# Optimization experiments

Measured on AMD Instinct MI355X. Metric: run time of the kernel, lower is better.

## Reference

```python
import jax, jax.numpy as jnp
import numpy as np
from jax import lax

NF, CF, LAT = 128, 3, 512          # n_filter, sobel c_factor (id+gx+gy), lat_size
NL, NC = 3, 4                      # n_layers (img 64 -> 3), n_calls
B, IMG, CH = 16, 64, 3
FIN, FH, FOUT = NF * CF, NF, 2 * NF  # dyna/res block in, hidden, out (gated -> 2*NF)
SPLIT = [NF, NF, NF, 1]
NOUT = sum(SPLIT)                  # 385
CS = NF + NF * 16 + NF * 16 + 16 * 16  # 4480 multi-cut state size
SEG = [FIN * FH, FH, FH * FH, FH, FH * FOUT, FOUT, FIN * FOUT, FOUT]
OFF = np.concatenate([[0], np.cumsum(SEG)]).astype(int)
K = int(OFF[-1])                   # hypernet output size (197376)

SOBEL_X = jnp.array([[-1., 0., 1.], [-2., 0., 2.], [-1., 0., 1.]], jnp.float32) / 8.0
SOBEL_Y = SOBEL_X.T
_g = np.exp(-0.5 * (np.arange(3) - 1.0) ** 2); _g /= _g.sum()
GAUSS = jnp.asarray(np.outer(_g, _g), jnp.float32)  # 3x3 gaussian, sigma=1


def dwconv(x, k2d):
    # depthwise conv, same 3x3 kernel for every channel, padding 1
    C = x.shape[1]
    k = jnp.broadcast_to(k2d.astype(x.dtype), (C, 1, 3, 3))
    return lax.conv_general_dilated(x, k, (1, 1), ((1, 1), (1, 1)),
                                    dimension_numbers=('NCHW', 'OIHW', 'NCHW'),
                                    feature_group_count=C)


def instnorm(x, eps=1e-5):
    m = x.mean((2, 3), keepdims=True)
    v = x.var((2, 3), keepdims=True)
    return (x - m) * lax.rsqrt(v + eps)


def conv1x1(x, w, b):  # w: [O, C]
    return jnp.einsum('bchw,oc->bohw', x, w) + b[None, :, None, None]


def lrb(x, w1, b1, w2, b2, wsc, bsc):  # LinearResidualBlock
    return x @ wsc.T + bsc + jax.nn.relu(x @ w1.T + b1) @ w2.T + b2


def _w(k, shape, fan_in):
    return jax.random.normal(k, shape, jnp.float32) / np.sqrt(fan_in)


def setup_inputs():
    ks = jax.random.split(jax.random.key(0), 24)
    z = lambda *s: jnp.zeros(s, jnp.float32)
    d = {}
    d['x'] = jax.random.normal(ks[0], (B, CH, IMG, IMG), jnp.float32)
    d['inj_lat'] = jax.random.normal(ks[1], (B, LAT), jnp.float32)
    d['leak_factor'] = jnp.float32(0.1)
    d['in_w'] = _w(ks[2], (NF, CH), CH); d['in_b'] = z(NF)
    d['fc_w1'] = _w(ks[3], (FH, FIN), FIN); d['fc_b1'] = z(FH)
    d['fc_w2'] = _w(ks[4], (FOUT, FH), FH); d['fc_b2'] = z(FOUT)
    d['fc_wsc'] = _w(ks[5], (FOUT, FIN), FIN); d['fc_bsc'] = z(FOUT)
    d['hyp_w'] = _w(ks[6], (K, LAT), LAT) * 0.1; d['hyp_b'] = z(K)
    d['lat_w'] = _w(ks[7], (NL * NC, LAT, LAT), LAT); d['lat_b'] = z(NL * NC, LAT)
    d['seed'] = _w(ks[8], (1, NF, 16, 16), NF)
    d['out_w'] = _w(ks[9], (NOUT, NF), NF); d['out_b'] = z(NOUT)
    d['l1_w1'] = _w(ks[10], (2 * LAT, CS), CS); d['l1_b1'] = z(2 * LAT)
    d['l1_w2'] = _w(ks[11], (LAT, 2 * LAT), 2 * LAT); d['l1_b2'] = z(LAT)
    d['l1_wsc'] = _w(ks[12], (LAT, CS), CS); d['l1_bsc'] = z(LAT)
    d['l2_w1'] = _w(ks[13], (LAT, LAT), LAT); d['l2_b1'] = z(LAT)
    d['l2_w2'] = _w(ks[14], (LAT, LAT), LAT); d['l2_b2'] = z(LAT)
    d['l2_wsc'] = _w(ks[15], (LAT, LAT), LAT); d['l2_bsc'] = z(LAT)
    d['fin_w'] = _w(ks[16], (LAT, LAT), LAT); d['fin_b'] = z(LAT)
    return d


def _forward(x, inj_lat, leak_factor, in_w, in_b, fc_w1, fc_b1, fc_w2, fc_b2,
             fc_wsc, fc_bsc, hyp_w, hyp_b, lat_w, lat_b, seed, out_w, out_b,
             l1_w1, l1_b1, l1_w2, l1_b2, l1_wsc, l1_bsc,
             l2_w1, l2_b1, l2_w2, l2_b2, l2_wsc, l2_bsc, fin_w, fin_b):
    out = conv1x1(x, in_w, in_b)
    leak = jnp.clip(leak_factor, 0.001, 1000.0)
    for c in range(NL * NC):
        # perception: identity + x/y sobel (c_factor=3), then instance norm
        p = jnp.concatenate([out, dwconv(out, SOBEL_X), dwconv(out, SOBEL_Y)], 1)
        p = instnorm(p)
        # static ResidualBlock (shared params)
        f = conv1x1(p, fc_wsc, fc_bsc) + conv1x1(jax.nn.relu(conv1x1(p, fc_w1, fc_b1)), fc_w2, fc_b2)
        # per-call latent expansion + hypernetwork -> per-sample 1x1 conv weights
        latc = inj_lat @ lat_w[c].T + lat_b[c]
        hk = latc @ hyp_w.T + hyp_b  # [B, K]
        w_in = hk[:, OFF[0]:OFF[1]].reshape(-1, FH, FIN); b_in = hk[:, OFF[1]:OFF[2]]
        w_md = hk[:, OFF[2]:OFF[3]].reshape(-1, FH, FH);  b_md = hk[:, OFF[3]:OFF[4]]
        w_ot = hk[:, OFF[4]:OFF[5]].reshape(-1, FOUT, FH); b_ot = hk[:, OFF[5]:OFF[6]]
        w_sc = hk[:, OFF[6]:OFF[7]].reshape(-1, FOUT, FIN); b_sc = hk[:, OFF[7]:OFF[8]]
        h = jax.nn.relu(jnp.einsum('bchw,boc->bohw', p, w_in) + b_in[:, :, None, None])
        h = jax.nn.relu(jnp.einsum('bchw,boc->bohw', h, w_md) + b_md[:, :, None, None])
        d = (jnp.einsum('bchw,boc->bohw', p, w_sc) + b_sc[:, :, None, None]
             + jnp.einsum('bchw,boc->bohw', h, w_ot) + b_ot[:, :, None, None])
        out_new = f + d  # [B, 2*NF, H, W]
        a, g = out_new[:, :NF], out_new[:, NF:]
        out = out + leak * (a * jax.nn.sigmoid(g))
        if c < NL * NC - 1 and c % NC == NC - 1:
            s = dwconv(out, GAUSS)
            # bilinear 0.5 downscale (align_corners=False) == 2x2 average
            Bn, C, H, W = s.shape
            out = s.reshape(Bn, C, H // 2, 2, W // 2, 2).mean((3, 5))
    out = out + seed  # broadcast seed [1, NF, 16, 16]
    o = conv1x1(out, out_w, out_b)  # [B, 385, 16, 16]
    f_, fh_, fw_, hw_ = o[:, :NF], o[:, NF:2 * NF], o[:, 2 * NF:3 * NF], o[:, 3 * NF:]
    bs = o.shape[0]
    cs = jnp.concatenate([f_.mean((2, 3)), fh_.mean(3).reshape(bs, -1),
                          fw_.mean(2).reshape(bs, -1), hw_.reshape(bs, -1)], 1)  # [B, 4480]
    hcs = lrb(cs, l1_w1, l1_b1, l1_w2, l1_b2, l1_wsc, l1_bsc)
    hcs = lrb(hcs, l2_w1, l2_b1, l2_w2, l2_b2, l2_wsc, l2_bsc)
    return hcs @ fin_w.T + fin_b  # [B, LAT]


def reference(x, inj_lat, leak_factor, in_w, in_b, fc_w1, fc_b1, fc_w2, fc_b2,
              fc_wsc, fc_bsc, hyp_w, hyp_b, lat_w, lat_b, seed, out_w, out_b,
              l1_w1, l1_b1, l1_w2, l1_b2, l1_wsc, l1_bsc,
              l2_w1, l2_b1, l2_w2, l2_b2, l2_wsc, l2_bsc, fin_w, fin_b):
    return _forward(x, inj_lat, leak_factor, in_w, in_b, fc_w1, fc_b1, fc_w2, fc_b2,
                    fc_wsc, fc_bsc, hyp_w, hyp_b, lat_w, lat_b, seed, out_w, out_b,
                    l1_w1, l1_b1, l1_w2, l1_b2, l1_wsc, l1_bsc,
                    l2_w1, l2_b1, l2_w2, l2_b2, l2_wsc, l2_bsc, fin_w, fin_b)
```

## Files before the change

### kernel.cpp

```cpp
#include <hip/hip_runtime.h>
#include <hip/hip_bf16.h>

typedef __hip_bfloat16 bf16;
typedef __attribute__((ext_vector_type(8))) short bf8_t;
typedef __attribute__((ext_vector_type(4))) float f4_t;

#define KHK 197376
#define OFF_WIN 0
#define OFF_BIN 49152
#define OFF_WMD 49280
#define OFF_BMD 65664
#define OFF_WOT 65792
#define OFF_BOT 98560
#define OFF_WSC 98816
#define OFF_BSC 197120

__device__ __forceinline__ float ldf(const float* p, size_t i){ return p[i]; }
__device__ __forceinline__ float ldf(const bf16* p, size_t i){ return __bfloat162float(p[i]); }
__device__ __forceinline__ void stf(float* p, size_t i, float v){ p[i] = v; }
__device__ __forceinline__ void stf(bf16* p, size_t i, float v){ p[i] = __float2bfloat16(v); }
__device__ __forceinline__ float b2f(short u){ return __uint_as_float(((unsigned)(unsigned short)u) << 16); }

typedef const __attribute__((address_space(1))) unsigned int* gas_t;
typedef __attribute__((address_space(3))) unsigned int* las_t;
__device__ __forceinline__ void gld_lds16(const void* g, void* l){
  __builtin_amdgcn_global_load_lds((gas_t)g, (las_t)l, 16, 0, 0);
}

struct Seg { const bf16* p; int klen; int ld; };

__global__ __launch_bounds__(256) void k_cvt_bf16(const float* __restrict__ in,
    bf16* __restrict__ out, size_t n){
  size_t stride = (size_t)gridDim.x * 256;
  for (size_t i = blockIdx.x*256ULL + threadIdx.x; i*8 < n; i += stride){
    float4 a = *reinterpret_cast<const float4*>(in + i*8);
    float4 c = *reinterpret_cast<const float4*>(in + i*8 + 4);
    union { bf8_t v; bf16 e[8]; } o;
    o.e[0]=__float2bfloat16(a.x); o.e[1]=__float2bfloat16(a.y);
    o.e[2]=__float2bfloat16(a.z); o.e[3]=__float2bfloat16(a.w);
    o.e[4]=__float2bfloat16(c.x); o.e[5]=__float2bfloat16(c.y);
    o.e[6]=__float2bfloat16(c.z); o.e[7]=__float2bfloat16(c.w);
    *reinterpret_cast<bf8_t*>(out + i*8) = o.v;
  }
}

__global__ __launch_bounds__(256) void k_in_conv(const float* __restrict__ x,
    const float* __restrict__ w, const float* __restrict__ b, float* __restrict__ out){
  int idx = blockIdx.x*256 + threadIdx.x;
  int c = idx & 127;
  int s = (idx >> 7) & 4095;
  int bi = idx >> 19;
  const float* xb = x + (size_t)bi*3*4096;
  out[idx] = b[c] + w[c*3]*xb[s] + w[c*3+1]*xb[4096+s] + w[c*3+2]*xb[8192+s];
}

__global__ __launch_bounds__(256) void k_sobel4(const float* __restrict__ src,
    bf16* __restrict__ p, int H, int S){
  int idx = blockIdx.x*256 + threadIdx.x;
  int c4 = (idx & 31) * 4;
  int s = (idx >> 5) % S;
  int b = idx / (S*32);
  int y = s / H, x = s - y*H;
  const float* sb = src + (size_t)b*S*128 + c4;
  float4 n[3][3];
  #pragma unroll
  for (int dy=0; dy<3; dy++)
    #pragma unroll
    for (int dx=0; dx<3; dx++){
      int yy = y + dy - 1, xx = x + dx - 1;
      if (yy>=0 && yy<H && xx>=0 && xx<H)
        n[dy][dx] = *reinterpret_cast<const float4*>(sb + (size_t)(yy*H+xx)*128);
      else
        n[dy][dx] = (float4){0.f,0.f,0.f,0.f};
    }
  float v0[4], sx[4], sy[4];
  #pragma unroll
  for (int q = 0; q < 4; q++){
    float e00=((const float*)&n[0][0])[q], e01=((const float*)&n[0][1])[q], e02=((const float*)&n[0][2])[q];
    float e10=((const float*)&n[1][0])[q], e11=((const float*)&n[1][1])[q], e12=((const float*)&n[1][2])[q];
    float e20=((const float*)&n[2][0])[q], e21=((const float*)&n[2][1])[q], e22=((const float*)&n[2][2])[q];
    v0[q] = e11;
    sx[q] = (-e00 + e02 - 2.f*e10 + 2.f*e12 - e20 + e22) * 0.125f;
    sy[q] = (-e00 - 2.f*e01 - e02 + e20 + 2.f*e21 + e22) * 0.125f;
  }
  bf16* pb = p + ((size_t)b*S + s)*384;
  union { unsigned long long u; bf16 e[4]; } o0, o1, o2;
  #pragma unroll
  for (int q = 0; q < 4; q++){
    o0.e[q] = __float2bfloat16(v0[q]);
    o1.e[q] = __float2bfloat16(sx[q]);
    o2.e[q] = __float2bfloat16(sy[q]);
  }
  *reinterpret_cast<unsigned long long*>(pb + c4)       = o0.u;
  *reinterpret_cast<unsigned long long*>(pb + 128 + c4) = o1.u;
  *reinterpret_cast<unsigned long long*>(pb + 256 + c4) = o2.u;
}

__global__ __launch_bounds__(256) void k_stats(const bf16* __restrict__ P_,
    float* __restrict__ SUMS, int S){
  __shared__ float sS[384], sQ[384];
  int b = blockIdx.y;
  int chunk = S >> 4;
  int s0 = blockIdx.x * chunk;
  int t = threadIdx.x;
  for (int i = t; i < 384; i += 256){ sS[i] = 0.f; sQ[i] = 0.f; }
  __syncthreads();
  if (t < 240){
    int oct = t % 48, ls = t / 48;
    int c8 = oct*8;
    float as[8] = {}, qs[8] = {};
    for (int s = s0 + ls; s < s0 + chunk; s += 5){
      bf8_t v = *reinterpret_cast<const bf8_t*>(P_ + ((size_t)b*S + s)*384 + c8);
      #pragma unroll
      for (int i=0;i<8;i++){ float f = b2f(v[i]); as[i]+=f; qs[i]+=f*f; }
    }
    #pragma unroll
    for (int i=0;i<8;i++){ atomicAdd(&sS[c8+i], as[i]); atomicAdd(&sQ[c8+i], qs[i]); }
  }
  __syncthreads();
  for (int i = t; i < 384; i += 256){
    atomicAdd(&SUMS[((size_t)b*384+i)*2],   sS[i]);
    atomicAdd(&SUMS[((size_t)b*384+i)*2+1], sQ[i]);
  }
}

__global__ __launch_bounds__(256) void k_hyper_all(const float* __restrict__ hw,
    const float* __restrict__ hb, const bf16* __restrict__ latb,
    bf16* __restrict__ hk_all){
  __shared__ float Sw[128][17];
  int h0 = blockIdx.x * 128;
  int tid = threadIdx.x, wid = tid >> 6, lane = tid & 63;
  int lr = lane & 15, lg = lane >> 4;
  f4_t acc[2][12];
  #pragma unroll
  for (int f=0; f<2; f++)
    #pragma unroll
    for (int j=0; j<12; j++) acc[f][j] = (f4_t){0.f,0.f,0.f,0.f};
  for (int k0 = 0; k0 < 512; k0 += 32){
    bf8_t af[2];
    #pragma unroll
    for (int f = 0; f < 2; f++){
      int h = h0 + wid*32 + f*16 + lr;
      const float* src = hw + (size_t)h*512 + k0 + lg*8;
      float4 x0 = *reinterpret_cast<const float4*>(src);
      float4 x1 = *reinterpret_cast<const float4*>(src + 4);
      union { bf8_t v; bf16 e[8]; } o;
      o.e[0]=__float2bfloat16(x0.x); o.e[1]=__float2bfloat16(x0.y);
      o.e[2]=__float2bfloat16(x0.z); o.e[3]=__float2bfloat16(x0.w);
      o.e[4]=__float2bfloat16(x1.x); o.e[5]=__float2bfloat16(x1.y);
      o.e[6]=__float2bfloat16(x1.z); o.e[7]=__float2bfloat16(x1.w);
      af[f] = o.v;
    }
    #pragma unroll
    for (int j = 0; j < 12; j++){
      bf8_t bv = *reinterpret_cast<const bf8_t*>(latb + (size_t)(j*16 + lr)*512 + k0 + lg*8);
      acc[0][j] = __builtin_amdgcn_mfma_f32_16x16x32_bf16(af[0], bv, acc[0][j], 0, 0, 0);
      acc[1][j] = __builtin_amdgcn_mfma_f32_16x16x32_bf16(af[1], bv, acc[1][j], 0, 0, 0);
    }
  }
  for (int j = 0; j < 12; j++){
    __syncthreads();
    #pragma unroll
    for (int f = 0; f < 2; f++)
      #pragma unroll
      for (int r = 0; r < 4; r++)
        Sw[wid*32 + f*16 + lg*4 + r][lr] = acc[f][j][r];
    __syncthreads();
    int bb = tid >> 4, h8 = (tid & 15) * 8;
    union { bf8_t v; bf16 e[8]; } o;
    #pragma unroll
    for (int i = 0; i < 8; i++)
      o.e[i] = __float2bfloat16(hb[h0 + h8 + i] + Sw[h8 + i][bb]);
    *reinterpret_cast<bf8_t*>(hk_all + ((size_t)j*16 + bb)*KHK + h0 + h8) = o.v;
  }
}

__global__ __launch_bounds__(256) void k_latall(const float* __restrict__ inj,
    const float* __restrict__ lat_w, const float* __restrict__ lat_b,
    bf16* __restrict__ LATB){
  int gwave = (int)((blockIdx.x*256 + threadIdx.x) >> 6);
  int lane = threadIdx.x & 63;
  int c = gwave >> 9, o = gwave & 511;
  const float* wr = lat_w + (size_t)c*262144 + (size_t)o*512;
  float acc[16] = {};
  for (int k = lane; k < 512; k += 64){
    float wv = wr[k];
    #pragma unroll
    for (int b = 0; b < 16; b++) acc[b] += wv * inj[b*512 + k];
  }
  #pragma unroll
  for (int b = 0; b < 16; b++)
    for (int off = 32; off > 0; off >>= 1) acc[b] += __shfl_down(acc[b], off);
  if (lane == 0){
    float bv = lat_b[c*512 + o];
    #pragma unroll
    for (int b = 0; b < 16; b++)
      LATB[(size_t)c*8192 + b*512 + o] = __float2bfloat16(acc[b] + bv);
  }
}

__global__ __launch_bounds__(256) void k_xform(
    const float* __restrict__ fc_w1, const float* __restrict__ fc_b1,
    const float* __restrict__ fc_w2, const float* __restrict__ fc_b2,
    const float* __restrict__ fc_wsc, const float* __restrict__ fc_bsc,
    const bf16* __restrict__ HK_, const float* __restrict__ SUMS, float Sf,
    bf16* __restrict__ Wstack, float* __restrict__ bstack,
    bf16* __restrict__ Wbig, float* __restrict__ bbig,
    bf16* __restrict__ Wmd, float* __restrict__ bmd){
  int gw = (blockIdx.x*256 + threadIdx.x) >> 6;
  int lane = threadIdx.x & 63;
  float invSf = 1.f / Sf;
  if (gw < 4096){
    int b = gw >> 8, o = gw & 255;
    const float* su = SUMS + (size_t)b*768;
    const bf16* hkb = HK_ + (size_t)b*KHK;
    float b0 = (o < 128) ? fc_b1[o] : ldf(hkb, OFF_BIN + (o-128));
    float accv = 0.f;
    bf16* dst = Wstack + ((size_t)b*256 + o)*384;
    for (int k = lane; k < 384; k += 64){
      float m = su[k*2] * invSf;
      float iv = rsqrtf(fmaxf(su[k*2+1]*invSf - m*m, 0.f) + 1e-5f);
      float wv = (o < 128) ? fc_w1[(size_t)o*384 + k]
                           : ldf(hkb, OFF_WIN + (size_t)(o-128)*384 + k);
      float w = wv * iv;
      accv += w * m;
      dst[k] = __float2bfloat16(w);
    }
    for (int off=32; off>0; off>>=1) accv += __shfl_down(accv, off);
    if (lane==0) bstack[b*256+o] = b0 - accv;
  } else if (gw < 8192){
    int r = gw - 4096; int b = r >> 8, o = r & 255;
    const float* su = SUMS + (size_t)b*768;
    const bf16* hkb = HK_ + (size_t)b*KHK;
    int cc = o & 127;
    int nr = ((cc >> 4) << 5) + ((o >> 7) << 4) + (cc & 15);
    bf16* dst = Wbig + ((size_t)b*256 + nr)*640;
    float accv = 0.f;
    for (int k = lane; k < 384; k += 64){
      float m = su[k*2] * invSf;
      float iv = rsqrtf(fmaxf(su[k*2+1]*invSf - m*m, 0.f) + 1e-5f);
      float w = (fc_wsc[(size_t)o*384 + k] + ldf(hkb, OFF_WSC + (size_t)o*384 + k)) * iv;
      accv += w * m;
      dst[k] = __float2bfloat16(w);
    }
    for (int k = lane; k < 128; k += 64){
      dst[384+k] = __float2bfloat16(fc_w2[(size_t)o*128 + k]);
      dst[512+k] = hkb[OFF_WOT + (size_t)o*128 + k];
    }
    for (int off=32; off>0; off>>=1) accv += __shfl_down(accv, off);
    if (lane==0) bbig[b*256+nr] = fc_bsc[o] + ldf(hkb, OFF_BSC+o) + fc_b2[o]
                                  + ldf(hkb, OFF_BOT+o) - accv;
  } else {
    int r = gw - 8192; int b = r >> 7, o = r & 127;
    const bf16* hkb = HK_ + (size_t)b*KHK;
    bf16* dst = Wmd + ((size_t)b*128 + o)*128;
    for (int k = lane; k < 128; k += 64)
      dst[k] = hkb[OFF_WMD + (size_t)o*128 + k];
    if (lane==0) bmd[b*128+o] = ldf(hkb, OFF_BMD + o);
  }
}

__global__ __launch_bounds__(512) void k_gemm1(const bf16* __restrict__ P_,
    const bf16* __restrict__ W, const float* __restrict__ bias,
    bf16* __restrict__ HGo, int S){
  __shared__ short As[128][32];
  __shared__ short Bs[256][32];
  int b = blockIdx.z, s0 = blockIdx.x * 128;
  int tid = threadIdx.x, wid = tid >> 6, lane = tid & 63;
  int wrow = (wid >> 2) * 64, wcol = (wid & 3) * 64;
  int lr = lane & 15, lg = lane >> 4;
  int r0 = tid >> 2, c8 = (tid & 3) * 8;
  const bf16* Wb = W + (size_t)b * 98304;
  f4_t acc[4][4] = {{}};
  const bf16* gA  = P_ + ((size_t)b*S + s0 + r0) * 384 + c8;
  const bf16* gB0 = Wb + (size_t)r0 * 384 + c8;
  const bf16* gB1 = Wb + (size_t)(128 + r0) * 384 + c8;
  for (int k0 = 0; k0 < 384; k0 += 32){
    gld_lds16(gA + k0,  &As[wid*16][0]);
    gld_lds16(gB0 + k0, &Bs[wid*16][0]);
    gld_lds16(gB1 + k0, &Bs[128 + wid*16][0]);
    __syncthreads();
    bf8_t af[4], bfv[4];
    #pragma unroll
    for (int i = 0; i < 4; i++) af[i]  = *(const bf8_t*)(&As[wrow + i*16 + lr][lg*8]);
    #pragma unroll
    for (int j = 0; j < 4; j++) bfv[j] = *(const bf8_t*)(&Bs[wcol + j*16 + lr][lg*8]);
    #pragma unroll
    for (int i = 0; i < 4; i++)
      #pragma unroll
      for (int j = 0; j < 4; j++)
        acc[i][j] = __builtin_amdgcn_mfma_f32_16x16x32_bf16(af[i], bfv[j], acc[i][j], 0, 0, 0);
    __syncthreads();
  }
  #pragma unroll
  for (int j = 0; j < 4; j++){
    int n = wcol + j*16 + lr;
    float bv = bias[(size_t)b * 256 + n];
    #pragma unroll
    for (int i = 0; i < 4; i++){
      int sr = s0 + wrow + i*16 + lg*4;
      size_t base = ((size_t)b * S + sr) * 256 + n;
      #pragma unroll
      for (int r = 0; r < 4; r++)
        stf(HGo, base + (size_t)r * 256, fmaxf(acc[i][j][r] + bv, 0.f));
    }
  }
}

__global__ __launch_bounds__(512) void k_gemm23(
    const bf16* __restrict__ P_, const bf16* __restrict__ HG_,
    const bf16* __restrict__ Wmd, const float* __restrict__ bmd,
    const bf16* __restrict__ Wbig, const float* __restrict__ bbig,
    float* __restrict__ OUTf, int S, const float* __restrict__ leakp){
  __shared__ short As[128][32];
  __shared__ short Bs[256][32];
  __shared__ short G2t[128][136];
  int b = blockIdx.z, s0 = blockIdx.x * 128;
  int tid = threadIdx.x, wid = tid >> 6, lane = tid & 63;
  int lr = lane & 15, lg = lane >> 4;
  int r0 = tid >> 2, c8 = (tid & 3) * 8;
  bf16* G2b = (bf16*)&G2t[0][0];
  {
    int wrowA = (wid >> 1) * 32, wcolA = (wid & 1) * 64;
    f4_t accA[2][4] = {{}};
    const bf16* gA = HG_ + ((size_t)b*S + s0 + r0) * 256 + 128 + c8;
    const bf16* gB = Wmd + (size_t)b*16384 + (size_t)r0 * 128 + c8;
    for (int k0 = 0; k0 < 128; k0 += 32){
      gld_lds16(gA + k0, &As[wid*16][0]);
      gld_lds16(gB + k0, &Bs[wid*16][0]);
      __syncthreads();
      bf8_t af[2], bfv[4];
      #pragma unroll
      for (int i = 0; i < 2; i++) af[i]  = *(const bf8_t*)(&As[wrowA + i*16 + lr][lg*8]);
      #pragma unroll
      for (int j = 0; j < 4; j++) bfv[j] = *(const bf8_t*)(&Bs[wcolA + j*16 + lr][lg*8]);
      #pragma unroll
      for (int i = 0; i < 2; i++)
        #pragma unroll
        for (int j = 0; j < 4; j++)
          accA[i][j] = __builtin_amdgcn_mfma_f32_16x16x32_bf16(af[i], bfv[j], accA[i][j], 0, 0, 0);
      __syncthreads();
    }
    const float* bmdb = bmd + b*128;
    #pragma unroll
    for (int j = 0; j < 4; j++){
      int col = wcolA + j*16 + lr;
      float bv = bmdb[col];
      #pragma unroll
      for (int i = 0; i < 2; i++){
        int row = wrowA + i*16 + lg*4;
        #pragma unroll
        for (int r = 0; r < 4; r++)
          stf(G2b, (size_t)(row + r)*136 + col, fmaxf(accA[i][j][r] + bv, 0.f));
      }
    }
    __syncthreads();
  }
  int wrow = (wid >> 2) * 64, wcol = (wid & 3) * 64;
  f4_t acc[4][4] = {{}};
  const bf16* Wb = Wbig + (size_t)b * 163840;
  {
    const bf16* gA  = P_ + ((size_t)b*S + s0 + r0) * 384 + c8;
    const bf16* gB0 = Wb + (size_t)r0 * 640 + c8;
    const bf16* gB1 = Wb + (size_t)(128 + r0) * 640 + c8;
    for (int k0 = 0; k0 < 384; k0 += 32){
      gld_lds16(gA + k0,  &As[wid*16][0]);
      gld_lds16(gB0 + k0, &Bs[wid*16][0]);
      gld_lds16(gB1 + k0, &Bs[128 + wid*16][0]);
      __syncthreads();
      bf8_t af[4], bfv[4];
      #pragma unroll
      for (int i = 0; i < 4; i++) af[i]  = *(const bf8_t*)(&As[wrow + i*16 + lr][lg*8]);
      #pragma unroll
      for (int j = 0; j < 4; j++) bfv[j] = *(const bf8_t*)(&Bs[wcol + j*16 + lr][lg*8]);
      #pragma unroll
      for (int i = 0; i < 4; i++)
        #pragma unroll
        for (int j = 0; j < 4; j++)
          acc[i][j] = __builtin_amdgcn_mfma_f32_16x16x32_bf16(af[i], bfv[j], acc[i][j], 0, 0, 0);
      __syncthreads();
    }
  }
  {
    const bf16* gA  = HG_ + ((size_t)b*S + s0 + r0) * 256 + c8;
    const bf16* gB0 = Wb + (size_t)r0 * 640 + 384 + c8;
    const bf16* gB1 = Wb + (size_t)(128 + r0) * 640 + 384 + c8;
    for (int k0 = 0; k0 < 128; k0 += 32){
      gld_lds16(gA + k0,  &As[wid*16][0]);
      gld_lds16(gB0 + k0, &Bs[wid*16][0]);
      gld_lds16(gB1 + k0, &Bs[128 + wid*16][0]);
      __syncthreads();
      bf8_t af[4], bfv[4];
      #pragma unroll
      for (int i = 0; i < 4; i++) af[i]  = *(const bf8_t*)(&As[wrow + i*16 + lr][lg*8]);
      #pragma unroll
      for (int j = 0; j < 4; j++) bfv[j] = *(const bf8_t*)(&Bs[wcol + j*16 + lr][lg*8]);
      #pragma unroll
      for (int i = 0; i < 4; i++)
        #pragma unroll
        for (int j = 0; j < 4; j++)
          acc[i][j] = __builtin_amdgcn_mfma_f32_16x16x32_bf16(af[i], bfv[j], acc[i][j], 0, 0, 0);
      __syncthreads();
    }
  }
  {
    const bf16* gB0 = Wb + (size_t)r0 * 640 + 512 + c8;
    const bf16* gB1 = Wb + (size_t)(128 + r0) * 640 + 512 + c8;
    for (int k0 = 0; k0 < 128; k0 += 32){
      gld_lds16(gB0 + k0, &Bs[wid*16][0]);
      gld_lds16(gB1 + k0, &Bs[128 + wid*16][0]);
      __syncthreads();
      bf8_t af[4], bfv[4];
      #pragma unroll
      for (int i = 0; i < 4; i++) af[i]  = *(const bf8_t*)(&G2t[wrow + i*16 + lr][k0 + lg*8]);
      #pragma unroll
      for (int j = 0; j < 4; j++) bfv[j] = *(const bf8_t*)(&Bs[wcol + j*16 + lr][lg*8]);
      #pragma unroll
      for (int i = 0; i < 4; i++)
        #pragma unroll
        for (int j = 0; j < 4; j++)
          acc[i][j] = __builtin_amdgcn_mfma_f32_16x16x32_bf16(af[i], bfv[j], acc[i][j], 0, 0, 0);
      __syncthreads();
    }
  }
  float leak = fminf(fmaxf(leakp[0], 0.001f), 1000.f);
  #pragma unroll
  for (int jp = 0; jp < 2; jp++){
    int na = wcol + jp*32 + lr;
    float bva = bbig[(size_t)b * 256 + na];
    float bvg = bbig[(size_t)b * 256 + na + 16];
    int chan = (wcol >> 1) + jp*16 + lr;
    #pragma unroll
    for (int i = 0; i < 4; i++){
      int sr = s0 + wrow + i*16 + lg*4;
      #pragma unroll
      for (int r = 0; r < 4; r++){
        float av = acc[i][jp*2][r]   + bva;
        float gv = acc[i][jp*2+1][r] + bvg;
        size_t oidx = ((size_t)b * S + sr + r) * 128 + chan;
        OUTf[oidx] += leak * av * (1.f / (1.f + expf(-gv)));
      }
    }
  }
}

template<int RELU, class TOUT>
__global__ __launch_bounds__(256) void k_mfgemm(
    Seg s1, const bf16* __restrict__ W, long long wbstride, int Ktot,
    const float* __restrict__ bias, int bbstride,
    TOUT* __restrict__ OUTp, int ldc, int Mout, int S){
  __shared__ short As[128][32];
  __shared__ short Bs[128][32];
  int b  = blockIdx.z;
  int s0 = blockIdx.x * 128;
  int n0 = blockIdx.y * 128;
  int tid = threadIdx.x;
  int wid = tid >> 6, lane = tid & 63;
  int wrow = (wid >> 1) * 64;
  int wcol = (wid & 1) * 64;
  int lr = lane & 15, lg = lane >> 4;
  int r0 = wid*32 + (lane >> 2);
  int c8 = (lane & 3) * 8;
  const bf16* Wb = W + (size_t)b * wbstride;
  f4_t acc[4][4] = {{}};
  const bf16* INb = s1.p + (size_t)b * S * s1.ld;
  const bf16* gA0 = INb + (size_t)(s0 + r0) * s1.ld + c8;
  const bf16* gA1 = INb + (size_t)(s0 + r0 + 16) * s1.ld + c8;
  const bf16* gB0 = Wb + (size_t)(n0 + r0) * Ktot + c8;
  const bf16* gB1 = Wb + (size_t)(n0 + r0 + 16) * Ktot + c8;
  for (int k0 = 0; k0 < s1.klen; k0 += 32){
    gld_lds16(gA0 + k0, &As[wid*32][0]);
    gld_lds16(gA1 + k0, &As[wid*32 + 16][0]);
    gld_lds16(gB0 + k0, &Bs[wid*32][0]);
    gld_lds16(gB1 + k0, &Bs[wid*32 + 16][0]);
    __syncthreads();
    bf8_t af[4], bfv[4];
    #pragma unroll
    for (int i = 0; i < 4; i++) af[i]  = *(const bf8_t*)(&As[wrow + i*16 + lr][lg*8]);
    #pragma unroll
    for (int j = 0; j < 4; j++) bfv[j] = *(const bf8_t*)(&Bs[wcol + j*16 + lr][lg*8]);
    #pragma unroll
    for (int i = 0; i < 4; i++)
      #pragma unroll
      for (int j = 0; j < 4; j++)
        acc[i][j] = __builtin_amdgcn_mfma_f32_16x16x32_bf16(af[i], bfv[j], acc[i][j], 0, 0, 0);
    __syncthreads();
  }
  #pragma unroll
  for (int j = 0; j < 4; j++){
    int n = n0 + wcol + j*16 + lr;
    if (n >= Mout) continue;
    float bv = bias[(size_t)b * bbstride + n];
    #pragma unroll
    for (int i = 0; i < 4; i++){
      int sr = s0 + wrow + i*16 + lg*4;
      size_t base = ((size_t)b * S + sr) * ldc + n;
      #pragma unroll
      for (int r = 0; r < 4; r++){
        float v = acc[i][j][r] + bv;
        if (RELU) v = fmaxf(v, 0.f);
        stf(OUTp, base + (size_t)r * ldc, v);
      }
    }
  }
}

__global__ __launch_bounds__(256) void k_blurpool(const float* __restrict__ src,
    float* __restrict__ dst, int H2, int S2){
  const float g[3] = {0.27406862f, 0.45186276f, 0.27406862f};
  int idx = blockIdx.x*256 + threadIdx.x;
  int c = idx & 127;
  int s2 = (idx >> 7) % S2;
  int b = idx / (S2*128);
  int y2 = s2 / H2, x2 = s2 - y2*H2;
  int H = H2*2;
  const float* sb = src + (size_t)b*(H*H)*128 + c;
  float acc = 0.f;
  #pragma unroll
  for (int dy2 = 0; dy2 < 2; dy2++)
    #pragma unroll
    for (int dx2 = 0; dx2 < 2; dx2++){
      int y = 2*y2 + dy2, x = 2*x2 + dx2;
      float bl = 0.f;
      #pragma unroll
      for (int i = 0; i < 3; i++)
        #pragma unroll
        for (int j = 0; j < 3; j++){
          int yy = y + i - 1, xx = x + j - 1;
          float v = (yy>=0 && yy<H && xx>=0 && xx<H) ? sb[(size_t)(yy*H+xx)*128] : 0.f;
          bl += v * g[i] * g[j];
        }
      acc += bl;
    }
  dst[idx] = acc * 0.25f;
}

__global__ __launch_bounds__(256) void k_seedcvt(const float* __restrict__ in,
    const float* __restrict__ seed, bf16* __restrict__ out){
  int idx = blockIdx.x*256 + threadIdx.x;
  int c = idx & 127;
  int s = (idx >> 7) & 255;
  out[idx] = __float2bfloat16(in[idx] + seed[c*256 + s]);
}

__global__ __launch_bounds__(256) void k_build_cs(const float* __restrict__ O,
    float* __restrict__ cs){
  int b = blockIdx.x;
  const float* Ob = O + (size_t)b*256*385;
  for (int id = threadIdx.x; id < 4480; id += 256){
    float v;
    if (id < 128){
      float s = 0; for (int t = 0; t < 256; t++) s += Ob[(size_t)t*385 + id];
      v = s * (1.f/256.f);
    } else if (id < 2176){
      int r = id - 128; int c = r >> 4, h = r & 15;
      float s = 0; for (int w = 0; w < 16; w++) s += Ob[(size_t)(h*16+w)*385 + 128 + c];
      v = s * (1.f/16.f);
    } else if (id < 4224){
      int r = id - 2176; int c = r >> 4, w = r & 15;
      float s = 0; for (int h = 0; h < 16; h++) s += Ob[(size_t)(h*16+w)*385 + 256 + c];
      v = s * (1.f/16.f);
    } else {
      v = Ob[(size_t)(id - 4224)*385 + 384];
    }
    cs[b*4480 + id] = v;
  }
}

template<int RELU, int ACCUM, class TOUT>
__global__ __launch_bounds__(256) void k_rowgemm(const float* __restrict__ IN,
    const float* __restrict__ W,
    const float* __restrict__ bias,
    TOUT* __restrict__ OUT, int M, int K){
  int wave = (int)((blockIdx.x*256 + threadIdx.x) >> 6);
  int lane = threadIdx.x & 63;
  if (wave >= M) return;
  const float* wr = W + (size_t)wave*K;
  float acc[16] = {};
  for (int k = lane; k < K; k += 64){
    float wv = wr[k];
    #pragma unroll
    for (int b = 0; b < 16; b++) acc[b] += wv * IN[b*K + k];
  }
  #pragma unroll
  for (int b = 0; b < 16; b++)
    for (int off = 32; off > 0; off >>= 1) acc[b] += __shfl_down(acc[b], off);
  if (lane == 0){
    float bv = bias[wave];
    #pragma unroll
    for (int b = 0; b < 16; b++){
      float v = acc[b] + bv;
      if (RELU) v = fmaxf(v, 0.f);
      size_t oi = (size_t)b*M + wave;
      if (ACCUM) v += ldf(OUT, oi);
      stf(OUT, oi, v);
    }
  }
}

template<int RELU1>
__global__ __launch_bounds__(256) void k_rowgemm2(const float* __restrict__ IN,
    const float* __restrict__ W1, const float* __restrict__ b1, float* __restrict__ O1, int M1,
    const float* __restrict__ W2, const float* __restrict__ b2, float* __restrict__ O2, int M2,
    int K){
  int wave = (int)((blockIdx.x*256 + threadIdx.x) >> 6);
  int lane = threadIdx.x & 63;
  if (wave >= M1 + M2) return;
  int second = (wave >= M1);
  int o = second ? (wave - M1) : wave;
  const float* wr = (second ? W2 : W1) + (size_t)o*K;
  float acc[16] = {};
  for (int k = lane; k < K; k += 64){
    float wv = wr[k];
    #pragma unroll
    for (int b = 0; b < 16; b++) acc[b] += wv * IN[b*K + k];
  }
  #pragma unroll
  for (int b = 0; b < 16; b++)
    for (int off = 32; off > 0; off >>= 1) acc[b] += __shfl_down(acc[b], off);
  if (lane == 0){
    float bv = second ? b2[o] : b1[o];
    float* OUT = second ? O2 : O1;
    int M = second ? M2 : M1;
    #pragma unroll
    for (int b = 0; b < 16; b++){
      float v = acc[b] + bv;
      if (RELU1 && !second) v = fmaxf(v, 0.f);
      OUT[(size_t)b*M + o] = v;
    }
  }
}

extern "C" void kernel_launch(void* const* d_in, const int* in_sizes, int n_in,
                              void* d_out, int out_size, void* d_ws, size_t ws_size,
                              hipStream_t stream){
  (void)in_sizes; (void)n_in; (void)out_size; (void)ws_size;
  const float* x      = (const float*)d_in[0];
  const float* inj    = (const float*)d_in[1];
  const float* leakp  = (const float*)d_in[2];
  const float* in_w   = (const float*)d_in[3];
  const float* in_b   = (const float*)d_in[4];
  const float* fc_w1  = (const float*)d_in[5];
  const float* fc_b1  = (const float*)d_in[6];
  const float* fc_w2  = (const float*)d_in[7];
  const float* fc_b2  = (const float*)d_in[8];
  const float* fc_wsc = (const float*)d_in[9];
  const float* fc_bsc = (const float*)d_in[10];
  const float* hyp_w  = (const float*)d_in[11];
  const float* hyp_b  = (const float*)d_in[12];
  const float* lat_w  = (const float*)d_in[13];
  const float* lat_b  = (const float*)d_in[14];
  const float* seed   = (const float*)d_in[15];
  const float* out_w  = (const float*)d_in[16];
  const float* out_b  = (const float*)d_in[17];
  const float* l1_w1  = (const float*)d_in[18];
  const float* l1_b1  = (const float*)d_in[19];
  const float* l1_w2  = (const float*)d_in[20];
  const float* l1_b2  = (const float*)d_in[21];
  const float* l1_wsc = (const float*)d_in[22];
  const float* l1_bsc = (const float*)d_in[23];
  const float* l2_w1  = (const float*)d_in[24];
  const float* l2_b1  = (const float*)d_in[25];
  const float* l2_w2  = (const float*)d_in[26];
  const float* l2_b2  = (const float*)d_in[27];
  const float* l2_wsc = (const float*)d_in[28];
  const float* l2_bsc = (const float*)d_in[29];
  const float* fin_w  = (const float*)d_in[30];
  const float* fin_b  = (const float*)d_in[31];

  char* ws = (char*)d_ws;
  float* OUT    = (float*)(ws);
  bf16*  P      = (bf16*)(ws + 33554432UL);
  bf16*  HG     = (bf16*)(ws + 83886080UL);
  bf16*  HKALL  = (bf16*)(ws + 134217728UL);
  bf16*  WSTK   = (bf16*)(ws + 285802496UL);
  bf16*  WBIG   = (bf16*)(ws + 288948224UL);
  bf16*  WMD    = (bf16*)(ws + 294191104UL);
  float* BSTK   = (float*)(ws + 294715392UL);
  float* BBIG   = (float*)(ws + 294731776UL);
  float* BMD    = (float*)(ws + 294748160UL);
  bf16*  LATB   = (bf16*)(ws + 294805504UL);
  bf16*  OUTB   = (bf16*)(ws + 295002112UL);
  float* OHEAD  = (float*)(ws + 296050688UL);
  bf16*  OWB    = (bf16*)(ws + 302358528UL);
  float* CS     = (float*)(ws + 302457088UL);
  float* T1     = (float*)(ws + 302743808UL);
  float* HCS    = (float*)(ws + 302809344UL);
  float* HCS2   = (float*)(ws + 302842112UL);
  float* SUMS12 = (float*)(ws + 302874880UL);
  float* OUT2   = (float*)(ws + 310378496UL);

  k_cvt_bf16<<<32, 256, 0, stream>>>(out_w, OWB, 49280ULL);
  k_in_conv<<<32768, 256, 0, stream>>>(x, in_w, in_b, OUT);

  k_latall<<<1536, 256, 0, stream>>>(inj, lat_w, lat_b, LATB);
  k_hyper_all<<<1542, 256, 0, stream>>>(hyp_w, hyp_b, LATB, HKALL);
  (void)hipMemsetAsync(SUMS12, 0, 12*16*384*2*sizeof(float), stream);

  float* cur = OUT;
  float* alt = OUT2;
  int H = 64;
  for (int c = 0; c < 12; c++){
    int S = H*H;
    float* SUMS = SUMS12 + (size_t)c*16*768;
    k_sobel4<<<(16*S*32)/256, 256, 0, stream>>>(cur, P, H, S);
    k_stats<<<dim3(16,16), 256, 0, stream>>>(P, SUMS, S);
    k_xform<<<2560, 256, 0, stream>>>(fc_w1, fc_b1, fc_w2, fc_b2, fc_wsc, fc_bsc,
                                      HKALL + (size_t)c*16*KHK, SUMS, (float)S,
                                      WSTK, BSTK, WBIG, BBIG, WMD, BMD);
    k_gemm1<<<dim3(S/128, 1, 16), 512, 0, stream>>>(P, WSTK, BSTK, HG, S);
    k_gemm23<<<dim3(S/128, 1, 16), 512, 0, stream>>>(
        P, HG, WMD, BMD, WBIG, BBIG, cur, S, leakp);
    if (c == 3 || c == 7){
      int H2 = H/2, S2 = S/4;
      k_blurpool<<<(16*S2*128)/256, 256, 0, stream>>>(cur, alt, H2, S2);
      float* t = cur; cur = alt; alt = t;
      H = H2;
    }
  }

  k_seedcvt<<<2048, 256, 0, stream>>>(cur, seed, OUTB);
  Seg segO = {OUTB, 128, 128};
  k_mfgemm<0,float><<<dim3(2, 4, 16), 256, 0, stream>>>(
      segO, OWB, 0LL, 128, out_b, 0, OHEAD, 385, 385, 256);
  k_build_cs<<<16, 256, 0, stream>>>(OHEAD, CS);

  k_rowgemm2<1><<<384, 256, 0, stream>>>(CS, l1_w1, l1_b1, T1, 1024,
                                         l1_wsc, l1_bsc, HCS, 512, 4480);
  k_rowgemm<0,1,float><<<128, 256, 0, stream>>>(T1, l1_w2, l1_b2, HCS, 512, 1024);
  k_rowgemm2<1><<<256, 256, 0, stream>>>(HCS, l2_w1, l2_b1, T1, 512,
                                         l2_wsc, l2_bsc, HCS2, 512, 512);
  k_rowgemm<0,1,float><<<128, 256, 0, stream>>>(T1, l2_w2, l2_b2, HCS2, 512, 512);
  k_rowgemm<0,0,float><<<128, 256, 0, stream>>>(HCS2, fin_w, fin_b, (float*)d_out, 512, 512);
}
```

Measured before the change: 1.500 ms.

## Fuse first-layer GEMM into cell GEMM kernel, keeping hidden activations in LDS

Measured after the change: 1.436 ms (median of 2 runs). 4.2% less time.

```diff
diff --git a/kernel.cpp b/kernel.cpp
--- a/kernel.cpp
+++ b/kernel.cpp
@@ -260,78 +260,72 @@
   }
 }
 
-__global__ __launch_bounds__(512) void k_gemm1(const bf16* __restrict__ P_,
-    const bf16* __restrict__ W, const float* __restrict__ bias,
-    bf16* __restrict__ HGo, int S){
-  __shared__ short As[128][32];
-  __shared__ short Bs[256][32];
-  int b = blockIdx.z, s0 = blockIdx.x * 128;
-  int tid = threadIdx.x, wid = tid >> 6, lane = tid & 63;
-  int wrow = (wid >> 2) * 64, wcol = (wid & 3) * 64;
-  int lr = lane & 15, lg = lane >> 4;
-  int r0 = tid >> 2, c8 = (tid & 3) * 8;
-  const bf16* Wb = W + (size_t)b * 98304;
-  f4_t acc[4][4] = {{}};
-  const bf16* gA  = P_ + ((size_t)b*S + s0 + r0) * 384 + c8;
-  const bf16* gB0 = Wb + (size_t)r0 * 384 + c8;
-  const bf16* gB1 = Wb + (size_t)(128 + r0) * 384 + c8;
-  for (int k0 = 0; k0 < 384; k0 += 32){
-    gld_lds16(gA + k0,  &As[wid*16][0]);
-    gld_lds16(gB0 + k0, &Bs[wid*16][0]);
-    gld_lds16(gB1 + k0, &Bs[128 + wid*16][0]);
-    __syncthreads();
-    bf8_t af[4], bfv[4];
-    #pragma unroll
-    for (int i = 0; i < 4; i++) af[i]  = *(const bf8_t*)(&As[wrow + i*16 + lr][lg*8]);
-    #pragma unroll
-    for (int j = 0; j < 4; j++) bfv[j] = *(const bf8_t*)(&Bs[wcol + j*16 + lr][lg*8]);
-    #pragma unroll
-    for (int i = 0; i < 4; i++)
-      #pragma unroll
-      for (int j = 0; j < 4; j++)
-        acc[i][j] = __builtin_amdgcn_mfma_f32_16x16x32_bf16(af[i], bfv[j], acc[i][j], 0, 0, 0);
-    __syncthreads();
-  }
-  #pragma unroll
-  for (int j = 0; j < 4; j++){
-    int n = wcol + j*16 + lr;
-    float bv = bias[(size_t)b * 256 + n];
-    #pragma unroll
-    for (int i = 0; i < 4; i++){
-      int sr = s0 + wrow + i*16 + lg*4;
-      size_t base = ((size_t)b * S + sr) * 256 + n;
-      #pragma unroll
-      for (int r = 0; r < 4; r++)
-        stf(HGo, base + (size_t)r * 256, fmaxf(acc[i][j][r] + bv, 0.f));
-    }
-  }
-}
-
-__global__ __launch_bounds__(512) void k_gemm23(
-    const bf16* __restrict__ P_, const bf16* __restrict__ HG_,
+__global__ __launch_bounds__(512) void k_cellgemm(
+    const bf16* __restrict__ P_,
+    const bf16* __restrict__ Wstk, const float* __restrict__ bstk,
     const bf16* __restrict__ Wmd, const float* __restrict__ bmd,
     const bf16* __restrict__ Wbig, const float* __restrict__ bbig,
     float* __restrict__ OUTf, int S, const float* __restrict__ leakp){
   __shared__ short As[128][32];
   __shared__ short Bs[256][32];
-  __shared__ short G2t[128][136];
+  __shared__ short H1t[128][136];
+  __shared__ short HmG[128][136];
   int b = blockIdx.z, s0 = blockIdx.x * 128;
   int tid = threadIdx.x, wid = tid >> 6, lane = tid & 63;
   int lr = lane & 15, lg = lane >> 4;
   int r0 = tid >> 2, c8 = (tid & 3) * 8;
-  bf16* G2b = (bf16*)&G2t[0][0];
+  bf16* H1b = (bf16*)&H1t[0][0];
+  bf16* HmGb = (bf16*)&HmG[0][0];
+  int wrow = (wid >> 2) * 64, wcol = (wid & 3) * 64;
+  f4_t acc[4][4] = {{}};
+  {
+    const bf16* gA  = P_ + ((size_t)b*S + s0 + r0) * 384 + c8;
+    const bf16* gB0 = Wstk + (size_t)b*98304 + (size_t)r0 * 384 + c8;
+    const bf16* gB1 = gB0 + (size_t)128 * 384;
+    for (int k0 = 0; k0 < 384; k0 += 32){
+      gld_lds16(gA + k0,  &As[wid*16][0]);
+      gld_lds16(gB0 + k0, &Bs[wid*16][0]);
+      gld_lds16(gB1 + k0, &Bs[128 + wid*16][0]);
+      __syncthreads();
+      bf8_t af[4], bfv[4];
+      #pragma unroll
+      for (int i = 0; i < 4; i++) af[i]  = *(const bf8_t*)(&As[wrow + i*16 + lr][lg*8]);
+      #pragma unroll
+      for (int j = 0; j < 4; j++) bfv[j] = *(const bf8_t*)(&Bs[wcol + j*16 + lr][lg*8]);
+      #pragma unroll
+      for (int i = 0; i < 4; i++)
+        #pragma unroll
+        for (int j = 0; j < 4; j++)
+          acc[i][j] = __builtin_amdgcn_mfma_f32_16x16x32_bf16(af[i], bfv[j], acc[i][j], 0, 0, 0);
+      __syncthreads();
+    }
+    #pragma unroll
+    for (int j = 0; j < 4; j++){
+      int n = wcol + j*16 + lr;
+      float bv = bstk[(size_t)b*256 + n];
+      bf16* dst = (n < 128) ? H1b : HmGb;
+      int col = n & 127;
+      #pragma unroll
+      for (int i = 0; i < 4; i++){
+        int row = wrow + i*16 + lg*4;
+        #pragma unroll
+        for (int r = 0; r < 4; r++)
+          stf(dst, (size_t)(row + r)*136 + col, fmaxf(acc[i][j][r] + bv, 0.f));
+      }
+    }
+    __syncthreads();
+  }
   {
     int wrowA = (wid >> 1) * 32, wcolA = (wid & 1) * 64;
     f4_t accA[2][4] = {{}};
-    const bf16* gA = HG_ + ((size_t)b*S + s0 + r0) * 256 + 128 + c8;
     const bf16* gB = Wmd + (size_t)b*16384 + (size_t)r0 * 128 + c8;
     for (int k0 = 0; k0 < 128; k0 += 32){
-      gld_lds16(gA + k0, &As[wid*16][0]);
       gld_lds16(gB + k0, &Bs[wid*16][0]);
       __syncthreads();
       bf8_t af[2], bfv[4];
       #pragma unroll
-      for (int i = 0; i < 2; i++) af[i]  = *(const bf8_t*)(&As[wrowA + i*16 + lr][lg*8]);
+      for (int i = 0; i < 2; i++)
+        af[i] = *(const bf8_t*)(&HmG[wrowA + i*16 + lr][k0 + lg*8]);
       #pragma unroll
       for (int j = 0; j < 4; j++) bfv[j] = *(const bf8_t*)(&Bs[wcolA + j*16 + lr][lg*8]);
       #pragma unroll
@@ -351,13 +345,16 @@
         int row = wrowA + i*16 + lg*4;
         #pragma unroll
         for (int r = 0; r < 4; r++)
-          stf(G2b, (size_t)(row + r)*136 + col, fmaxf(accA[i][j][r] + bv, 0.f));
+          stf(HmGb, (size_t)(row + r)*136 + col, fmaxf(accA[i][j][r] + bv, 0.f));
       }
     }
     __syncthreads();
   }
-  int wrow = (wid >> 2) * 64, wcol = (wid & 3) * 64;
-  f4_t acc[4][4] = {{}};
+  #pragma unroll
+  for (int i = 0; i < 4; i++)
+    #pragma unroll
+    for (int j = 0; j < 4; j++)
+      acc[i][j] = (f4_t){0.f,0.f,0.f,0.f};
   const bf16* Wb = Wbig + (size_t)b * 163840;
   {
     const bf16* gA  = P_ + ((size_t)b*S + s0 + r0) * 384 + c8;
@@ -382,17 +379,15 @@
     }
   }
   {
-    const bf16* gA  = HG_ + ((size_t)b*S + s0 + r0) * 256 + c8;
     const bf16* gB0 = Wb + (size_t)r0 * 640 + 384 + c8;
     const bf16* gB1 = Wb + (size_t)(128 + r0) * 640 + 384 + c8;
     for (int k0 = 0; k0 < 128; k0 += 32){
-      gld_lds16(gA + k0,  &As[wid*16][0]);
       gld_lds16(gB0 + k0, &Bs[wid*16][0]);
       gld_lds16(gB1 + k0, &Bs[128 + wid*16][0]);
       __syncthreads();
       bf8_t af[4], bfv[4];
       #pragma unroll
-      for (int i = 0; i < 4; i++) af[i]  = *(const bf8_t*)(&As[wrow + i*16 + lr][lg*8]);
+      for (int i = 0; i < 4; i++) af[i]  = *(const bf8_t*)(&H1t[wrow + i*16 + lr][k0 + lg*8]);
       #pragma unroll
       for (int j = 0; j < 4; j++) bfv[j] = *(const bf8_t*)(&Bs[wcol + j*16 + lr][lg*8]);
       #pragma unroll
@@ -412,7 +407,7 @@
       __syncthreads();
       bf8_t af[4], bfv[4];
       #pragma unroll
-      for (int i = 0; i < 4; i++) af[i]  = *(const bf8_t*)(&G2t[wrow + i*16 + lr][k0 + lg*8]);
+      for (int i = 0; i < 4; i++) af[i]  = *(const bf8_t*)(&HmG[wrow + i*16 + lr][k0 + lg*8]);
       #pragma unroll
       for (int j = 0; j < 4; j++) bfv[j] = *(const bf8_t*)(&Bs[wcol + j*16 + lr][lg*8]);
       #pragma unroll
@@ -671,7 +666,6 @@
   char* ws = (char*)d_ws;
   float* OUT    = (float*)(ws);
   bf16*  P      = (bf16*)(ws + 33554432UL);
-  bf16*  HG     = (bf16*)(ws + 83886080UL);
   bf16*  HKALL  = (bf16*)(ws + 134217728UL);
   bf16*  WSTK   = (bf16*)(ws + 285802496UL);
   bf16*  WBIG   = (bf16*)(ws + 288948224UL);
@@ -708,9 +702,8 @@
     k_xform<<<2560, 256, 0, stream>>>(fc_w1, fc_b1, fc_w2, fc_b2, fc_wsc, fc_bsc,
                                       HKALL + (size_t)c*16*KHK, SUMS, (float)S,
                                       WSTK, BSTK, WBIG, BBIG, WMD, BMD);
-    k_gemm1<<<dim3(S/128, 1, 16), 512, 0, stream>>>(P, WSTK, BSTK, HG, S);
-    k_gemm23<<<dim3(S/128, 1, 16), 512, 0, stream>>>(
-        P, HG, WMD, BMD, WBIG, BBIG, cur, S, leakp);
+    k_cellgemm<<<dim3(S/128, 1, 16), 512, 0, stream>>>(
+        P, WSTK, BSTK, WMD, BMD, WBIG, BBIG, cur, S, leakp);
     if (c == 3 || c == 7){
       int H2 = H/2, S2 = S/4;
       k_blurpool<<<(16*S2*128)/256, 256, 0, stream>>>(cur, alt, H2, S2);
```
